# Kernel optimization log

Hardware: AMD Instinct MI355X
Metric: run time of the kernel (lower is better)

The kernel has to match this reference:

```python
import jax, jax.numpy as jnp
import numpy as np

# Config matching init_kwargs
DILS = [1, 3, 6, 12]          # flattened dilations for blocks [[1,3],[6,12]]
BLOCK_START = [0, 2]          # layer index where each block starts
IN = 64                       # input_size
SS = 256                      # state_size
HS = 128                      # h_size
OS = SS - HS                  # out_size for S2Cell
OUT = 8                       # output_size
B = 1024                      # batch (number of series)
T = 256                       # timesteps
# per-layer lxh input widths: [in, out, out+in, out] each + 2*h
IN_SIZES = [IN + 2 * HS, OS + 2 * HS, OS + IN + 2 * HS, OS + 2 * HS]


def setup_inputs() -> dict:
    key = jax.random.key(0)
    ks = jax.random.split(key, 12)
    d = {"x": jax.random.normal(ks[0], (T, B, IN), jnp.float32)}
    for i in range(4):
        fan_in = IN_SIZES[i]
        d[f"W{i}"] = jax.random.normal(ks[1 + i], (4 * SS, fan_in), jnp.float32) / np.sqrt(fan_in)
        d[f"b{i}"] = jnp.zeros((4 * SS,), jnp.float32)
    d["Wout"] = jax.random.normal(ks[9], (OUT, OS), jnp.float32) / np.sqrt(OS)
    d["bout"] = jnp.zeros((OUT,), jnp.float32)
    return d


def _s2cell(t, inp, W, b, prevH, prevC, bufH, bufC, dil):
    """One S2Cell step. bufH/bufC are circular buffers of length dil holding
    states from the last `dil` steps; bufH[t % dil] is the state from t-dil."""
    idx = t % dil
    has_del = t >= dil
    dH = jnp.where(has_del, bufH[idx], prevH)   # [B, HS]
    dC = bufC[idx]                               # [B, SS] (only used when has_del)
    xh = jnp.concatenate([inp, prevH, dH], axis=1)
    gates = xh @ W.T + b                         # [B, 4*SS]
    g0, g1, g2, g3 = jnp.split(gates, 4, axis=1)
    forget = jax.nn.sigmoid(g0 + 1.0)
    cand = jnp.tanh(g1)
    alpha = jax.nn.sigmoid(g2)
    out_gate = jax.nn.sigmoid(g3)
    weightedC = jnp.where(has_del, alpha * prevC + (1.0 - alpha) * dC, prevC)
    newC = jnp.where(t >= 1, forget * weightedC + (1.0 - forget) * cand, cand)
    whole = out_gate * newC                      # [B, SS]
    out_t, h = whole[:, :OS], whole[:, OS:]
    return out_t, h, newC, bufH.at[idx].set(h), bufC.at[idx].set(newC)


def reference(x, W0, b0, W1, b1, W2, b2, W3, b3, Wout, bout):
    Ws = [W0, W1, W2, W3]
    bs = [b0, b1, b2, b3]

    def init_layer(d):
        return (jnp.zeros((B, HS), x.dtype), jnp.zeros((B, SS), x.dtype),
                jnp.zeros((d, B, HS), x.dtype), jnp.zeros((d, B, SS), x.dtype))

    carry0 = (jnp.int32(0), tuple(init_layer(d) for d in DILS))

    def step(carry, x_t):
        t, states = carry
        new_states = []
        inp = x_t
        for li in range(4):
            if li in BLOCK_START and li > 0:
                # first layer of a later block: cat(previous block output, original input)
                inp = jnp.concatenate([inp, x_t], axis=1)
            prevH, prevC, bufH, bufC = states[li]
            inp, h, c, bufH, bufC = _s2cell(t, inp, Ws[li], bs[li], prevH, prevC, bufH, bufC, DILS[li])
            new_states.append((h, c, bufH, bufC))
        y = inp @ Wout.T + bout
        return (t + 1, tuple(new_states)), y

    _, ys = jax.lax.scan(step, carry0, x)
    return ys  # [T, B, OUT]
```

## Files before the change

kernel.cpp:

```cpp
#include <hip/hip_runtime.h>
#include <stdint.h>
#include <stdio.h>


typedef __attribute__((ext_vector_type(8))) short short8;
typedef __attribute__((ext_vector_type(4))) float f32x4;

#define DEVINL static __device__ __forceinline__

constexpr int TT = 256, BBATCH = 1024, INW = 64, HSW = 128, OSW = 128, NO = 8;
constexpr int ROWS = 128;

constexpr int KLa[4]   = {192, 384, 448, 384};
constexpr int DILa[4]  = {1, 3, 6, 12};
constexpr int PERa[4]  = {2, 4, 7, 13};
constexpr int LDWa[4]  = {200, 392, 456, 392};
constexpr int WOFFa[4] = {0, 6400, 18944, 33536};

constexpr int BIAS_B  = 46080 * 2;
constexpr int WOUT_B  = BIAS_B + 128 * 4;
constexpr int WSTR    = 129;
constexpr int BOUT_B  = WOUT_B + 8 * WSTR * 4;
constexpr int C3_B    = BOUT_B + 32;
constexpr int C3STR   = 132;
constexpr int LDS_BYTES = C3_B + 96 * C3STR * 4;

constexpr size_t WSBASE    = 8192;
constexpr size_t BH_OFF[4] = {0, 65536, 196608, 425984};
constexpr size_t OUTB_OFF  = 851968;
constexpr size_t CB_OFF    = 983040;
constexpr size_t C1_SZ     = 393216;
constexpr size_t C2_SZ     = 786432;
constexpr size_t CLSZ      = CB_OFF + C1_SZ + C2_SZ;
constexpr size_t WS_NEED   = WSBASE + 8 * CLSZ;

__host__ __device__ constexpr int seg_type(int L, int k) {
  if (L == 0) return k < 64 ? 0 : 2;
  if (L == 1) return k < 128 ? 1 : (k < 256 ? 2 : 3);
  if (L == 2) return k < 128 ? 1 : (k < 192 ? 0 : (k < 320 ? 2 : 3));
  return k < 128 ? 1 : (k < 256 ? 2 : 3);
}
__host__ __device__ constexpr int seg_start(int L, int k) {
  if (L == 0) return k < 64 ? 0 : 64;
  if (L == 1) return k < 128 ? 0 : (k < 256 ? 128 : 256);
  if (L == 2) return k < 128 ? 0 : (k < 192 ? 128 : (k < 320 ? 192 : 320));
  return k < 128 ? 0 : (k < 256 ? 128 : 256);
}

template <int N> struct IC { static constexpr int value = N; };

DEVINL unsigned short f2bf(float f) {
  union { float f; uint32_t u; } v; v.f = f;
  return (unsigned short)((v.u + 0x7FFFu + ((v.u >> 16) & 1u)) >> 16);
}
DEVINL float bf2f(unsigned short h) {
  union { uint32_t u; float f; } v; v.u = ((uint32_t)h) << 16;
  return v.f;
}
DEVINL float sigm(float x)  { return 1.0f / (1.0f + __expf(-x)); }
DEVINL float tanh_(float x) { return 1.0f - 2.0f / (__expf(2.0f * x) + 1.0f); }

DEVINL short8 zero_s8() { short8 v; for (int i = 0; i < 8; i++) v[i] = 0; return v; }
DEVINL f32x4  zero_f4() { f32x4  v; for (int i = 0; i < 4; i++) v[i] = 0.f; return v; }

DEVINL f32x4 mfma16(short8 a, short8 b, f32x4 c) {
  return __builtin_amdgcn_mfma_f32_16x16x32_bf16(a, b, c, 0, 0, 0);
}

DEVINL short8 ld8f(const float* p) {
  const f32x4 u0 = *(const f32x4*)p;
  const f32x4 u1 = *(const f32x4*)(p + 4);
  short8 r;
  r[0] = (short)f2bf(u0[0]); r[1] = (short)f2bf(u0[1]);
  r[2] = (short)f2bf(u0[2]); r[3] = (short)f2bf(u0[3]);
  r[4] = (short)f2bf(u1[0]); r[5] = (short)f2bf(u1[1]);
  r[6] = (short)f2bf(u1[2]); r[7] = (short)f2bf(u1[3]);
  return r;
}

__global__ void __launch_bounds__(256, 1)
rnn_stack_kernel(const float* __restrict__ x,
                 const float* __restrict__ W0, const float* __restrict__ b0,
                 const float* __restrict__ W1, const float* __restrict__ b1,
                 const float* __restrict__ W2, const float* __restrict__ b2,
                 const float* __restrict__ W3, const float* __restrict__ b3,
                 const float* __restrict__ Wout, const float* __restrict__ bout,
                 float* __restrict__ yout, char* __restrict__ ws)
{
  extern __shared__ char smem[];
  unsigned short* wlds = (unsigned short*)smem;
  float* biasl = (float*)(smem + BIAS_B);
  float* woutl = (float*)(smem + WOUT_B);
  float* boutl = (float*)(smem + BOUT_B);
  float* c3l   = (float*)(smem + C3_B);

  const int tid = threadIdx.x;

  __shared__ unsigned s_cg;
  if (tid == 0) {
    unsigned xcc;
    asm volatile("s_getreg_b32 %0, hwreg(HW_REG_XCC_ID)" : "=s"(xcc));
    xcc &= 7u;
    unsigned rank = __hip_atomic_fetch_add(
        (unsigned*)(ws + 4096 + (size_t)xcc * 64), 1u,
        __ATOMIC_RELAXED, __HIP_MEMORY_SCOPE_AGENT);
    s_cg = (xcc << 8) | (rank & 31u);
  }
  __syncthreads();
  const int c = __builtin_amdgcn_readfirstlane((int)(s_cg >> 8));
  const int g = __builtin_amdgcn_readfirstlane((int)(s_cg & 255));

  char* cb = ws + WSBASE + (size_t)c * CLSZ;
  unsigned short* bufH[4];
  unsigned short* outb[4];
#pragma unroll
  for (int l = 0; l < 4; l++) {
    bufH[l] = (unsigned short*)(cb + BH_OFF[l]);
    outb[l] = (unsigned short*)(cb + OUTB_OFF + (size_t)l * ROWS * OSW * 2);
  }
  float* bufC1 = (float*)(cb + CB_OFF + (size_t)g * (3 * 8 * ROWS * 4));
  float* bufC2 = (float*)(cb + CB_OFF + C1_SZ + (size_t)g * (6 * 8 * ROWS * 4));

  {
    const float* Wsrc[4] = {W0, W1, W2, W3};
    const float* bsrc[4] = {b0, b1, b2, b3};
    for (int l = 0; l < 4; l++) {
      const int K = KLa[l], LDW = LDWa[l];
      const int Ksrc = (l == 0) ? 320 : K;
      for (int n = 0; n < 32; n++) {
        const int grow = (n >> 3) * 256 + g * 8 + (n & 7);
        const float* src = Wsrc[l] + (size_t)grow * Ksrc;
        unsigned short* dst = wlds + WOFFa[l] + n * LDW;
        for (int k = tid; k < K; k += 256) {
          float v = src[k];
          if (l == 0 && k >= 64) v += src[k + 128];
          dst[k] = f2bf(v);
        }
      }
      if (tid < 32) biasl[l * 32 + tid] = bsrc[l][(tid >> 3) * 256 + g * 8 + (tid & 7)];
    }
    for (int i = tid; i < 8 * 128; i += 256) woutl[(i >> 7) * WSTR + (i & 127)] = Wout[i];
    if (tid < 8) boutl[tid] = bout[tid];
  }
  __syncthreads();

  const int wv = tid >> 6, lane = tid & 63, lm = lane & 15, quad = lane >> 4;
  const int m0 = wv * 32;
  const bool hi = lm >= 8;
  const int j = lm & 7;
  const int mrow = m0 + (hi ? 16 : 0) + quad * 4;

  unsigned* flg = (unsigned*)(ws + (size_t)c * 512 + (size_t)wv * 128);

  f32x4 pc[4];
#pragma unroll
  for (int l = 0; l < 4; l++) pc[l] = zero_f4();

  f32x4 acc00, acc01, acc10, acc11;

  auto arrive = [&](unsigned ep) {
    asm volatile("s_waitcnt vmcnt(0)" ::: "memory");
    if (lane == 0)
      __hip_atomic_store(flg + g, ep, __ATOMIC_RELAXED, __HIP_MEMORY_SCOPE_AGENT);
  };
  auto waitbar = [&](unsigned ep) {
    asm volatile("" ::: "memory");
    for (;;) {
      unsigned v = __hip_atomic_load(flg + (lane & 31), __ATOMIC_RELAXED,
                                     __HIP_MEMORY_SCOPE_AGENT);
      if (__all((int)(v >= ep))) break;
      __builtin_amdgcn_s_sleep(1);
    }
    asm volatile("buffer_inv sc0" ::: "memory");
  };

  auto pre = [&](auto Lc, int t) {
    constexpr int L = decltype(Lc)::value;
    constexpr int K = KLa[L];
    constexpr int NKT = K / 32;
    constexpr int DL = DILa[L];
    constexpr int P = PERa[L];
    constexpr int LDW = LDWa[L];
    const unsigned short* wl = wlds + WOFFa[L];
    const float bb0 = biasl[L * 32 + lm] + (lm < 8 ? 1.0f : 0.0f);
    const float bb1 = biasl[L * 32 + 16 + lm];
    acc00 = (f32x4){bb0, bb0, bb0, bb0};
    acc10 = acc00;
    acc01 = (f32x4){bb1, bb1, bb1, bb1};
    acc11 = acc01;
    const unsigned short* phb =
        (t >= 1) ? bufH[L] + (size_t)((t - 1) % P) * ROWS * HSW : nullptr;
    const unsigned short* dhb =
        (t >= DL) ? bufH[L] + (size_t)((t - DL) % P) * ROWS * HSW : phb;
    const float* xb = x + ((size_t)t * BBATCH + (size_t)c * ROWS) * INW;
#pragma unroll
    for (int kt = 0; kt < NKT; kt++) {
      const int sty = seg_type(L, kt * 32);
      if (sty == 1) continue;
      const int sst = seg_start(L, kt * 32);
      const int kloc = kt * 32 - sst + quad * 8;
      short8 a0, a1;
      if (sty == 0) {
        const float* p = xb + (size_t)(m0 + lm) * INW + kloc;
        a0 = ld8f(p);
        a1 = ld8f(p + 16 * INW);
      } else {
        const unsigned short* sb = (sty == 2) ? phb : dhb;
        if (sb) {
          const unsigned short* p = sb + (size_t)(m0 + lm) * HSW + kloc;
          a0 = *(const short8*)p;
          a1 = *(const short8*)(p + 16 * HSW);
        } else {
          a0 = zero_s8();
          a1 = zero_s8();
        }
      }
      const short8 bf0 = *(const short8*)(wl + (size_t)lm * LDW + kt * 32 + quad * 8);
      const short8 bf1 = *(const short8*)(wl + (size_t)(16 + lm) * LDW + kt * 32 + quad * 8);
      acc00 = mfma16(a0, bf0, acc00);
      acc01 = mfma16(a0, bf1, acc01);
      acc10 = mfma16(a1, bf0, acc10);
      acc11 = mfma16(a1, bf1, acc11);
    }
  };

  auto post = [&](auto Lc, int t) {
    constexpr int L = decltype(Lc)::value;
    constexpr int K = KLa[L];
    constexpr int NKT = K / 32;
    constexpr int DL = DILa[L];
    constexpr int P = PERa[L];
    constexpr int LDW = LDWa[L];
    if constexpr (L > 0) {
      const unsigned short* wl = wlds + WOFFa[L];
      const unsigned short* ob = outb[L - 1];
#pragma unroll
      for (int kt = 0; kt < NKT; kt++) {
        if (seg_type(L, kt * 32) != 1) continue;
        const int kloc = kt * 32 + quad * 8;
        const unsigned short* p = ob + (size_t)(m0 + lm) * HSW + kloc;
        const short8 a0 = *(const short8*)p;
        const short8 a1 = *(const short8*)(p + 16 * HSW);
        const short8 bf0 = *(const short8*)(wl + (size_t)lm * LDW + kt * 32 + quad * 8);
        const short8 bf1 = *(const short8*)(wl + (size_t)(16 + lm) * LDW + kt * 32 + quad * 8);
        acc00 = mfma16(a0, bf0, acc00);
        acc01 = mfma16(a0, bf1, acc01);
        acc10 = mfma16(a1, bf0, acc10);
        acc11 = mfma16(a1, bf1, acc11);
      }
    }
    f32x4 s00, s01, s10, s11;
#pragma unroll
    for (int r = 0; r < 4; r++) {
      s00[r] = __shfl_xor(acc00[r], 8);
      s01[r] = __shfl_xor(acc01[r], 8);
      s10[r] = __shfl_xor(acc10[r], 8);
      s11[r] = __shfl_xor(acc11[r], 8);
    }
    f32x4 G0, G1, G2, G3;
#pragma unroll
    for (int r = 0; r < 4; r++) {
      G0[r] = hi ? s10[r] : acc00[r];
      G1[r] = hi ? acc10[r] : s00[r];
      G2[r] = hi ? s11[r] : acc01[r];
      G3[r] = hi ? acc11[r] : s01[r];
    }
    float* cs = nullptr;
    if constexpr (L == 1) cs = bufC1 + ((size_t)(t % 3) * 8 + j) * ROWS + mrow;
    if constexpr (L == 2) cs = bufC2 + ((size_t)(t % 6) * 8 + j) * ROWS + mrow;
    float* cs3 = nullptr;
    if constexpr (L == 3) cs3 = c3l + ((size_t)(t % 12) * 8 + j) * C3STR + mrow;
    f32x4 dC = zero_f4();
    if constexpr (L == 1 || L == 2) { if (t >= DL) dC = *(const f32x4*)cs; }
    if constexpr (L == 3)           { if (t >= DL) dC = *(const f32x4*)cs3; }
    const f32x4 pcv = pc[L];
    f32x4 nC, wh;
#pragma unroll
    for (int q = 0; q < 4; q++) {
      const float fg = sigm(G0[q]);
      const float cd = tanh_(G1[q]);
      const float og = sigm(G3[q]);
      float wc;
      if constexpr (L == 0) {
        wc = pcv[q];
      } else {
        const float al = sigm(G2[q]);
        wc = (t >= DL) ? (al * pcv[q] + (1.0f - al) * dC[q]) : pcv[q];
      }
      const float nc = (t >= 1) ? (fg * wc + (1.0f - fg) * cd) : cd;
      nC[q] = nc;
      wh[q] = og * nc;
    }
    if constexpr (L == 1 || L == 2) *(f32x4*)cs = nC;
    if constexpr (L == 3)           *(f32x4*)cs3 = nC;
    pc[L] = nC;
    const int jg = g * 8 + j;
#pragma unroll
    for (int r = 0; r < 4; r++) {
      const unsigned short us = f2bf(wh[r]);
      const int row = mrow + r;
      if (g < 16) outb[L][(size_t)row * OSW + jg] = us;
      else bufH[L][((size_t)(t % P) * ROWS + row) * HSW + (jg - 128)] = us;
    }
  };

  auto epilogue = [&](int tt) {
    const int r = m0 + g;
    const unsigned short* orow = outb[3] + (size_t)r * OSW;
    const int o = lane >> 3, s = lane & 7;
    const short8 v0 = *(const short8*)(orow + s * 16);
    const short8 v1 = *(const short8*)(orow + s * 16 + 8);
    float part = 0.f;
#pragma unroll
    for (int i = 0; i < 8; i++)
      part += bf2f((unsigned short)v0[i]) * woutl[o * WSTR + s * 16 + i];
#pragma unroll
    for (int i = 0; i < 8; i++)
      part += bf2f((unsigned short)v1[i]) * woutl[o * WSTR + s * 16 + 8 + i];
    part += __shfl_down(part, 4);
    part += __shfl_down(part, 2);
    part += __shfl_down(part, 1);
    if (s == 0)
      yout[((size_t)tt * BBATCH + (size_t)c * ROWS + r) * NO + o] = part + boutl[o];
  };

  pre(IC<0>{}, 0);
  for (int t = 0; t < TT; t++) {
    const unsigned pb = 4u * t;
    post(IC<0>{}, t); arrive(pb + 1); pre(IC<1>{}, t);
    if (t > 0) epilogue(t - 1);
    waitbar(pb + 1);
    post(IC<1>{}, t); arrive(pb + 2); pre(IC<2>{}, t); waitbar(pb + 2);
    post(IC<2>{}, t); arrive(pb + 3); pre(IC<3>{}, t); waitbar(pb + 3);
    post(IC<3>{}, t); arrive(pb + 4);
    if (t + 1 < TT) pre(IC<0>{}, t + 1);
    waitbar(pb + 4);
  }
  epilogue(TT - 1);
}

extern "C" void kernel_launch(void* const* d_in, const int* in_sizes, int n_in,
                              void* d_out, int out_size, void* d_ws, size_t ws_size,
                              hipStream_t stream) {
  const float* x    = (const float*)d_in[0];
  const float* W0   = (const float*)d_in[1];
  const float* b0   = (const float*)d_in[2];
  const float* W1   = (const float*)d_in[3];
  const float* b1   = (const float*)d_in[4];
  const float* W2   = (const float*)d_in[5];
  const float* b2   = (const float*)d_in[6];
  const float* W3   = (const float*)d_in[7];
  const float* b3   = (const float*)d_in[8];
  const float* Wout = (const float*)d_in[9];
  const float* bout = (const float*)d_in[10];
  float* out = (float*)d_out;
  char* ws = (char*)d_ws;

  if (ws_size < WS_NEED) {
    fprintf(stderr, "kernel_launch: ws_size %zu < needed %zu\n", ws_size, (size_t)WS_NEED);
    return;
  }

  hipMemsetAsync(d_ws, 0, 8192, stream);

  hipError_t e = hipFuncSetAttribute((const void*)rnn_stack_kernel,
                                     hipFuncAttributeMaxDynamicSharedMemorySize,
                                     LDS_BYTES);
  if (e != hipSuccess) fprintf(stderr, "hipFuncSetAttribute: %d\n", (int)e);

  rnn_stack_kernel<<<dim3(256), dim3(256), LDS_BYTES, stream>>>(
      x, W0, b0, W1, b1, W2, b2, W3, b3, Wout, bout, out, ws);
  e = hipGetLastError();
  if (e != hipSuccess) fprintf(stderr, "launch error: %d\n", (int)e);
}
```

Baseline: 4.493 ms.

## Wavefront-pipeline layers across timesteps with one barrier per step

Replaces the four grid-wide barriers per timestep with a diagonal wavefront schedule. Layer L at step s processes timestep s-L, so all four layers run between a single barrier and cross-layer outputs are double-buffered by timestep parity. It also retiles the LDS weight layout into contiguous MFMA fragment blocks and changes the C-state buffers to per-thread contiguous float4 slots. Each barrier interval now carries more serial work, and the prologue and epilogue add three extra pipeline steps.

```diff
diff --git a/kernel.cpp b/kernel.cpp
--- a/kernel.cpp
+++ b/kernel.cpp
@@ -14,23 +14,22 @@
 constexpr int KLa[4]   = {192, 384, 448, 384};
 constexpr int DILa[4]  = {1, 3, 6, 12};
 constexpr int PERa[4]  = {2, 4, 7, 13};
-constexpr int LDWa[4]  = {200, 392, 456, 392};
-constexpr int WOFFa[4] = {0, 6400, 18944, 33536};
-
-constexpr int BIAS_B  = 46080 * 2;
-constexpr int WOUT_B  = BIAS_B + 128 * 4;
+constexpr int WOFFa[4] = {0, 6144, 18432, 32768};
+constexpr int WBYTES   = 90112;
+
+constexpr int BIAS_B  = WBYTES;
+constexpr int WOUT_B  = BIAS_B + 512;
 constexpr int WSTR    = 129;
 constexpr int BOUT_B  = WOUT_B + 8 * WSTR * 4;
 constexpr int C3_B    = BOUT_B + 32;
-constexpr int C3STR   = 132;
-constexpr int LDS_BYTES = C3_B + 96 * C3STR * 4;
+constexpr int LDS_BYTES = C3_B + 12 * 256 * 16;
 
 constexpr size_t WSBASE    = 8192;
 constexpr size_t BH_OFF[4] = {0, 65536, 196608, 425984};
 constexpr size_t OUTB_OFF  = 851968;
-constexpr size_t CB_OFF    = 983040;
-constexpr size_t C1_SZ     = 393216;
-constexpr size_t C2_SZ     = 786432;
+constexpr size_t CB_OFF    = OUTB_OFF + 8 * 32768;
+constexpr size_t C1_SZ     = 32 * 3 * 256 * 16;
+constexpr size_t C2_SZ     = 32 * 6 * 256 * 16;
 constexpr size_t CLSZ      = CB_OFF + C1_SZ + C2_SZ;
 constexpr size_t WS_NEED   = WSBASE + 8 * CLSZ;
 
@@ -112,29 +111,31 @@
 
   char* cb = ws + WSBASE + (size_t)c * CLSZ;
   unsigned short* bufH[4];
-  unsigned short* outb[4];
+  unsigned short* outb[8];
 #pragma unroll
   for (int l = 0; l < 4; l++) {
     bufH[l] = (unsigned short*)(cb + BH_OFF[l]);
-    outb[l] = (unsigned short*)(cb + OUTB_OFF + (size_t)l * ROWS * OSW * 2);
-  }
-  float* bufC1 = (float*)(cb + CB_OFF + (size_t)g * (3 * 8 * ROWS * 4));
-  float* bufC2 = (float*)(cb + CB_OFF + C1_SZ + (size_t)g * (6 * 8 * ROWS * 4));
+    outb[l * 2]     = (unsigned short*)(cb + OUTB_OFF + (size_t)(l * 2) * ROWS * OSW * 2);
+    outb[l * 2 + 1] = (unsigned short*)(cb + OUTB_OFF + (size_t)(l * 2 + 1) * ROWS * OSW * 2);
+  }
+  float* bufC1 = (float*)(cb + CB_OFF + (size_t)g * (3 * 256 * 16));
+  float* bufC2 = (float*)(cb + CB_OFF + C1_SZ + (size_t)g * (6 * 256 * 16));
 
   {
     const float* Wsrc[4] = {W0, W1, W2, W3};
     const float* bsrc[4] = {b0, b1, b2, b3};
     for (int l = 0; l < 4; l++) {
-      const int K = KLa[l], LDW = LDWa[l];
+      const int K = KLa[l];
       const int Ksrc = (l == 0) ? 320 : K;
+      unsigned short* base = wlds + WOFFa[l];
       for (int n = 0; n < 32; n++) {
         const int grow = (n >> 3) * 256 + g * 8 + (n & 7);
         const float* src = Wsrc[l] + (size_t)grow * Ksrc;
-        unsigned short* dst = wlds + WOFFa[l] + n * LDW;
         for (int k = tid; k < K; k += 256) {
           float v = src[k];
           if (l == 0 && k >= 64) v += src[k + 128];
-          dst[k] = f2bf(v);
+          base[((k >> 5) * 2 + (n >> 4)) * 512 + (n & 15) * 32 +
+               ((k >> 3) & 3) * 8 + (k & 7)] = f2bf(v);
         }
       }
       if (tid < 32) biasl[l * 32 + tid] = bsrc[l][(tid >> 3) * 256 + g * 8 + (tid & 7)];
@@ -155,8 +156,6 @@
   f32x4 pc[4];
 #pragma unroll
   for (int l = 0; l < 4; l++) pc[l] = zero_f4();
-
-  f32x4 acc00, acc01, acc10, acc11;
 
   auto arrive = [&](unsigned ep) {
     asm volatile("s_waitcnt vmcnt(0)" ::: "memory");
@@ -174,29 +173,35 @@
     asm volatile("buffer_inv sc0" ::: "memory");
   };
 
-  auto pre = [&](auto Lc, int t) {
+  auto do_layer = [&](auto Lc, int t) {
     constexpr int L = decltype(Lc)::value;
     constexpr int K = KLa[L];
     constexpr int NKT = K / 32;
     constexpr int DL = DILa[L];
     constexpr int P = PERa[L];
-    constexpr int LDW = LDWa[L];
+    if (t < 0 || t >= TT) return;
     const unsigned short* wl = wlds + WOFFa[L];
     const float bb0 = biasl[L * 32 + lm] + (lm < 8 ? 1.0f : 0.0f);
     const float bb1 = biasl[L * 32 + 16 + lm];
-    acc00 = (f32x4){bb0, bb0, bb0, bb0};
-    acc10 = acc00;
-    acc01 = (f32x4){bb1, bb1, bb1, bb1};
-    acc11 = acc01;
+    f32x4 acc00 = (f32x4){bb0, bb0, bb0, bb0};
+    f32x4 acc10 = acc00;
+    f32x4 acc01 = (f32x4){bb1, bb1, bb1, bb1};
+    f32x4 acc11 = acc01;
     const unsigned short* phb =
         (t >= 1) ? bufH[L] + (size_t)((t - 1) % P) * ROWS * HSW : nullptr;
     const unsigned short* dhb =
         (t >= DL) ? bufH[L] + (size_t)((t - DL) % P) * ROWS * HSW : phb;
+    const unsigned short* ob = (L > 0) ? outb[(L - 1) * 2 + (t & 1)] : nullptr;
     const float* xb = x + ((size_t)t * BBATCH + (size_t)c * ROWS) * INW;
+
+    f32x4 dC = zero_f4();
+    if constexpr (L == 1) { if (t >= DL) dC = *(const f32x4*)(bufC1 + ((size_t)(t % 3) * 256 + tid) * 4); }
+    if constexpr (L == 2) { if (t >= DL) dC = *(const f32x4*)(bufC2 + ((size_t)(t % 6) * 256 + tid) * 4); }
+    if constexpr (L == 3) { if (t >= DL) dC = *(const f32x4*)(c3l + ((size_t)(t % 12) * 256 + tid) * 4); }
+
 #pragma unroll
     for (int kt = 0; kt < NKT; kt++) {
       const int sty = seg_type(L, kt * 32);
-      if (sty == 1) continue;
       const int sst = seg_start(L, kt * 32);
       const int kloc = kt * 32 - sst + quad * 8;
       short8 a0, a1;
@@ -204,6 +209,10 @@
         const float* p = xb + (size_t)(m0 + lm) * INW + kloc;
         a0 = ld8f(p);
         a1 = ld8f(p + 16 * INW);
+      } else if (sty == 1) {
+        const unsigned short* p = ob + (size_t)(m0 + lm) * HSW + kloc;
+        a0 = *(const short8*)p;
+        a1 = *(const short8*)(p + 16 * HSW);
       } else {
         const unsigned short* sb = (sty == 2) ? phb : dhb;
         if (sb) {
@@ -215,39 +224,12 @@
           a1 = zero_s8();
         }
       }
-      const short8 bf0 = *(const short8*)(wl + (size_t)lm * LDW + kt * 32 + quad * 8);
-      const short8 bf1 = *(const short8*)(wl + (size_t)(16 + lm) * LDW + kt * 32 + quad * 8);
+      const short8 bf0 = *(const short8*)(wl + (kt * 2 + 0) * 512 + lm * 32 + quad * 8);
+      const short8 bf1 = *(const short8*)(wl + (kt * 2 + 1) * 512 + lm * 32 + quad * 8);
       acc00 = mfma16(a0, bf0, acc00);
       acc01 = mfma16(a0, bf1, acc01);
       acc10 = mfma16(a1, bf0, acc10);
       acc11 = mfma16(a1, bf1, acc11);
-    }
-  };
-
-  auto post = [&](auto Lc, int t) {
-    constexpr int L = decltype(Lc)::value;
-    constexpr int K = KLa[L];
-    constexpr int NKT = K / 32;
-    constexpr int DL = DILa[L];
-    constexpr int P = PERa[L];
-    constexpr int LDW = LDWa[L];
-    if constexpr (L > 0) {
-      const unsigned short* wl = wlds + WOFFa[L];
-      const unsigned short* ob = outb[L - 1];
-#pragma unroll
-      for (int kt = 0; kt < NKT; kt++) {
-        if (seg_type(L, kt * 32) != 1) continue;
-        const int kloc = kt * 32 + quad * 8;
-        const unsigned short* p = ob + (size_t)(m0 + lm) * HSW + kloc;
-        const short8 a0 = *(const short8*)p;
-        const short8 a1 = *(const short8*)(p + 16 * HSW);
-        const short8 bf0 = *(const short8*)(wl + (size_t)lm * LDW + kt * 32 + quad * 8);
-        const short8 bf1 = *(const short8*)(wl + (size_t)(16 + lm) * LDW + kt * 32 + quad * 8);
-        acc00 = mfma16(a0, bf0, acc00);
-        acc01 = mfma16(a0, bf1, acc01);
-        acc10 = mfma16(a1, bf0, acc10);
-        acc11 = mfma16(a1, bf1, acc11);
-      }
     }
     f32x4 s00, s01, s10, s11;
 #pragma unroll
@@ -265,14 +247,6 @@
       G2[r] = hi ? s11[r] : acc01[r];
       G3[r] = hi ? acc11[r] : s01[r];
     }
-    float* cs = nullptr;
-    if constexpr (L == 1) cs = bufC1 + ((size_t)(t % 3) * 8 + j) * ROWS + mrow;
-    if constexpr (L == 2) cs = bufC2 + ((size_t)(t % 6) * 8 + j) * ROWS + mrow;
-    float* cs3 = nullptr;
-    if constexpr (L == 3) cs3 = c3l + ((size_t)(t % 12) * 8 + j) * C3STR + mrow;
-    f32x4 dC = zero_f4();
-    if constexpr (L == 1 || L == 2) { if (t >= DL) dC = *(const f32x4*)cs; }
-    if constexpr (L == 3)           { if (t >= DL) dC = *(const f32x4*)cs3; }
     const f32x4 pcv = pc[L];
     f32x4 nC, wh;
 #pragma unroll
@@ -291,22 +265,24 @@
       nC[q] = nc;
       wh[q] = og * nc;
     }
-    if constexpr (L == 1 || L == 2) *(f32x4*)cs = nC;
-    if constexpr (L == 3)           *(f32x4*)cs3 = nC;
+    if constexpr (L == 1) *(f32x4*)(bufC1 + ((size_t)(t % 3) * 256 + tid) * 4) = nC;
+    if constexpr (L == 2) *(f32x4*)(bufC2 + ((size_t)(t % 6) * 256 + tid) * 4) = nC;
+    if constexpr (L == 3) *(f32x4*)(c3l + ((size_t)(t % 12) * 256 + tid) * 4) = nC;
     pc[L] = nC;
     const int jg = g * 8 + j;
+    unsigned short* outw = outb[L * 2 + (t & 1)];
 #pragma unroll
     for (int r = 0; r < 4; r++) {
       const unsigned short us = f2bf(wh[r]);
       const int row = mrow + r;
-      if (g < 16) outb[L][(size_t)row * OSW + jg] = us;
+      if (g < 16) outw[(size_t)row * OSW + jg] = us;
       else bufH[L][((size_t)(t % P) * ROWS + row) * HSW + (jg - 128)] = us;
     }
   };
 
   auto epilogue = [&](int tt) {
     const int r = m0 + g;
-    const unsigned short* orow = outb[3] + (size_t)r * OSW;
+    const unsigned short* orow = outb[3 * 2 + (tt & 1)] + (size_t)r * OSW;
     const int o = lane >> 3, s = lane & 7;
     const short8 v0 = *(const short8*)(orow + s * 16);
     const short8 v1 = *(const short8*)(orow + s * 16 + 8);
@@ -324,17 +300,14 @@
       yout[((size_t)tt * BBATCH + (size_t)c * ROWS + r) * NO + o] = part + boutl[o];
   };
 
-  pre(IC<0>{}, 0);
-  for (int t = 0; t < TT; t++) {
-    const unsigned pb = 4u * t;
-    post(IC<0>{}, t); arrive(pb + 1); pre(IC<1>{}, t);
-    if (t > 0) epilogue(t - 1);
-    waitbar(pb + 1);
-    post(IC<1>{}, t); arrive(pb + 2); pre(IC<2>{}, t); waitbar(pb + 2);
-    post(IC<2>{}, t); arrive(pb + 3); pre(IC<3>{}, t); waitbar(pb + 3);
-    post(IC<3>{}, t); arrive(pb + 4);
-    if (t + 1 < TT) pre(IC<0>{}, t + 1);
-    waitbar(pb + 4);
+  for (int s = 0; s < TT + 3; s++) {
+    do_layer(IC<0>{}, s);
+    do_layer(IC<1>{}, s - 1);
+    do_layer(IC<2>{}, s - 2);
+    do_layer(IC<3>{}, s - 3);
+    if (s >= 4) epilogue(s - 4);
+    arrive((unsigned)(s + 1));
+    waitbar((unsigned)(s + 1));
   }
   epilogue(TT - 1);
 }
```

Result: slower. 5.641 ms (+25.5%).

## Double waves per block, split rows per wave and swizzle LDS weight layout

Applied to the files above, without the earlier changes.

Launches 512 threads per block instead of 256, so each wave owns 16 batch rows instead of 32 and issues half the MFMAs per step. This shortens the serial per-step critical path. Weights are stored in LDS in an MFMA-fragment-tiled layout rather than a padded row-major layout, and the cell-state buffers are reorganised into per-lane float4 slots. The A fragments and the delayed C are loaded up front, and the gate math now runs only on half the lanes. In exchange the grid barrier has more waves to synchronise and flag polling, and half the lanes sit idle during the elementwise step.

```diff
diff --git a/kernel.cpp b/kernel.cpp
--- a/kernel.cpp
+++ b/kernel.cpp
@@ -14,23 +14,22 @@
 constexpr int KLa[4]   = {192, 384, 448, 384};
 constexpr int DILa[4]  = {1, 3, 6, 12};
 constexpr int PERa[4]  = {2, 4, 7, 13};
-constexpr int LDWa[4]  = {200, 392, 456, 392};
-constexpr int WOFFa[4] = {0, 6400, 18944, 33536};
-
-constexpr int BIAS_B  = 46080 * 2;
-constexpr int WOUT_B  = BIAS_B + 128 * 4;
+constexpr int WOFFa[4] = {0, 6144, 18432, 32768};
+constexpr int WBYTES   = 90112;
+
+constexpr int BIAS_B  = WBYTES;
+constexpr int WOUT_B  = BIAS_B + 512;
 constexpr int WSTR    = 129;
 constexpr int BOUT_B  = WOUT_B + 8 * WSTR * 4;
 constexpr int C3_B    = BOUT_B + 32;
-constexpr int C3STR   = 132;
-constexpr int LDS_BYTES = C3_B + 96 * C3STR * 4;
-
-constexpr size_t WSBASE    = 8192;
+constexpr int LDS_BYTES = C3_B + 12 * 256 * 16;
+
+constexpr size_t WSBASE    = 16384;
 constexpr size_t BH_OFF[4] = {0, 65536, 196608, 425984};
 constexpr size_t OUTB_OFF  = 851968;
 constexpr size_t CB_OFF    = 983040;
-constexpr size_t C1_SZ     = 393216;
-constexpr size_t C2_SZ     = 786432;
+constexpr size_t C1_SZ     = 32 * 3 * 256 * 16;
+constexpr size_t C2_SZ     = 32 * 6 * 256 * 16;
 constexpr size_t CLSZ      = CB_OFF + C1_SZ + C2_SZ;
 constexpr size_t WS_NEED   = WSBASE + 8 * CLSZ;
 
@@ -78,7 +77,7 @@
   return r;
 }
 
-__global__ void __launch_bounds__(256, 1)
+__global__ void __launch_bounds__(512, 1)
 rnn_stack_kernel(const float* __restrict__ x,
                  const float* __restrict__ W0, const float* __restrict__ b0,
                  const float* __restrict__ W1, const float* __restrict__ b1,
@@ -102,7 +101,7 @@
     asm volatile("s_getreg_b32 %0, hwreg(HW_REG_XCC_ID)" : "=s"(xcc));
     xcc &= 7u;
     unsigned rank = __hip_atomic_fetch_add(
-        (unsigned*)(ws + 4096 + (size_t)xcc * 64), 1u,
+        (unsigned*)(ws + 8192 + (size_t)xcc * 64), 1u,
         __ATOMIC_RELAXED, __HIP_MEMORY_SCOPE_AGENT);
     s_cg = (xcc << 8) | (rank & 31u);
   }
@@ -118,45 +117,47 @@
     bufH[l] = (unsigned short*)(cb + BH_OFF[l]);
     outb[l] = (unsigned short*)(cb + OUTB_OFF + (size_t)l * ROWS * OSW * 2);
   }
-  float* bufC1 = (float*)(cb + CB_OFF + (size_t)g * (3 * 8 * ROWS * 4));
-  float* bufC2 = (float*)(cb + CB_OFF + C1_SZ + (size_t)g * (6 * 8 * ROWS * 4));
+  float* bufC1 = (float*)(cb + CB_OFF + (size_t)g * (3 * 256 * 16));
+  float* bufC2 = (float*)(cb + CB_OFF + C1_SZ + (size_t)g * (6 * 256 * 16));
 
   {
     const float* Wsrc[4] = {W0, W1, W2, W3};
     const float* bsrc[4] = {b0, b1, b2, b3};
     for (int l = 0; l < 4; l++) {
-      const int K = KLa[l], LDW = LDWa[l];
+      const int K = KLa[l];
       const int Ksrc = (l == 0) ? 320 : K;
+      unsigned short* base = wlds + WOFFa[l];
       for (int n = 0; n < 32; n++) {
         const int grow = (n >> 3) * 256 + g * 8 + (n & 7);
         const float* src = Wsrc[l] + (size_t)grow * Ksrc;
-        unsigned short* dst = wlds + WOFFa[l] + n * LDW;
-        for (int k = tid; k < K; k += 256) {
+        for (int k = tid; k < K; k += 512) {
           float v = src[k];
           if (l == 0 && k >= 64) v += src[k + 128];
-          dst[k] = f2bf(v);
+          base[((k >> 5) * 2 + (n >> 4)) * 512 + (n & 15) * 32 +
+               ((k >> 3) & 3) * 8 + (k & 7)] = f2bf(v);
         }
       }
       if (tid < 32) biasl[l * 32 + tid] = bsrc[l][(tid >> 3) * 256 + g * 8 + (tid & 7)];
     }
-    for (int i = tid; i < 8 * 128; i += 256) woutl[(i >> 7) * WSTR + (i & 127)] = Wout[i];
+    for (int i = tid; i < 8 * 128; i += 512) woutl[(i >> 7) * WSTR + (i & 127)] = Wout[i];
     if (tid < 8) boutl[tid] = bout[tid];
   }
   __syncthreads();
 
   const int wv = tid >> 6, lane = tid & 63, lm = lane & 15, quad = lane >> 4;
-  const int m0 = wv * 32;
-  const bool hi = lm >= 8;
+  const int m0 = wv * 16;
   const int j = lm & 7;
-  const int mrow = m0 + (hi ? 16 : 0) + quad * 4;
-
-  unsigned* flg = (unsigned*)(ws + (size_t)c * 512 + (size_t)wv * 128);
+  const int mrow = m0 + quad * 4;
+  const int oid = wv * 32 + quad * 8 + j;
+
+  unsigned* flg = (unsigned*)(ws + (size_t)c * 1024 + (size_t)wv * 128);
 
   f32x4 pc[4];
 #pragma unroll
   for (int l = 0; l < 4; l++) pc[l] = zero_f4();
 
-  f32x4 acc00, acc01, acc10, acc11;
+  f32x4 acc0, acc1;
+  f32x4 dCreg = zero_f4();
 
   auto arrive = [&](unsigned ep) {
     asm volatile("s_waitcnt vmcnt(0)" ::: "memory");
@@ -180,132 +181,107 @@
     constexpr int NKT = K / 32;
     constexpr int DL = DILa[L];
     constexpr int P = PERa[L];
-    constexpr int LDW = LDWa[L];
     const unsigned short* wl = wlds + WOFFa[L];
     const float bb0 = biasl[L * 32 + lm] + (lm < 8 ? 1.0f : 0.0f);
     const float bb1 = biasl[L * 32 + 16 + lm];
-    acc00 = (f32x4){bb0, bb0, bb0, bb0};
-    acc10 = acc00;
-    acc01 = (f32x4){bb1, bb1, bb1, bb1};
-    acc11 = acc01;
+    acc0 = (f32x4){bb0, bb0, bb0, bb0};
+    acc1 = (f32x4){bb1, bb1, bb1, bb1};
+    dCreg = zero_f4();
+    if constexpr (L == 1) { if (t >= DL) dCreg = *(const f32x4*)(bufC1 + ((size_t)(t % 3) * 256 + oid) * 4); }
+    if constexpr (L == 2) { if (t >= DL) dCreg = *(const f32x4*)(bufC2 + ((size_t)(t % 6) * 256 + oid) * 4); }
+    if constexpr (L == 3) { if (t >= DL) dCreg = *(const f32x4*)(c3l + ((size_t)(t % 12) * 256 + oid) * 4); }
     const unsigned short* phb =
         (t >= 1) ? bufH[L] + (size_t)((t - 1) % P) * ROWS * HSW : nullptr;
     const unsigned short* dhb =
         (t >= DL) ? bufH[L] + (size_t)((t - DL) % P) * ROWS * HSW : phb;
     const float* xb = x + ((size_t)t * BBATCH + (size_t)c * ROWS) * INW;
+    short8 af[NKT];
 #pragma unroll
     for (int kt = 0; kt < NKT; kt++) {
       const int sty = seg_type(L, kt * 32);
       if (sty == 1) continue;
       const int sst = seg_start(L, kt * 32);
       const int kloc = kt * 32 - sst + quad * 8;
-      short8 a0, a1;
       if (sty == 0) {
-        const float* p = xb + (size_t)(m0 + lm) * INW + kloc;
-        a0 = ld8f(p);
-        a1 = ld8f(p + 16 * INW);
+        af[kt] = ld8f(xb + (size_t)(m0 + lm) * INW + kloc);
       } else {
         const unsigned short* sb = (sty == 2) ? phb : dhb;
-        if (sb) {
-          const unsigned short* p = sb + (size_t)(m0 + lm) * HSW + kloc;
-          a0 = *(const short8*)p;
-          a1 = *(const short8*)(p + 16 * HSW);
-        } else {
-          a0 = zero_s8();
-          a1 = zero_s8();
-        }
-      }
-      const short8 bf0 = *(const short8*)(wl + (size_t)lm * LDW + kt * 32 + quad * 8);
-      const short8 bf1 = *(const short8*)(wl + (size_t)(16 + lm) * LDW + kt * 32 + quad * 8);
-      acc00 = mfma16(a0, bf0, acc00);
-      acc01 = mfma16(a0, bf1, acc01);
-      acc10 = mfma16(a1, bf0, acc10);
-      acc11 = mfma16(a1, bf1, acc11);
+        af[kt] = sb ? *(const short8*)(sb + (size_t)(m0 + lm) * HSW + kloc)
+                    : zero_s8();
+      }
+    }
+#pragma unroll
+    for (int kt = 0; kt < NKT; kt++) {
+      if (seg_type(L, kt * 32) == 1) continue;
+      const short8 bf0v = *(const short8*)(wl + (kt * 2 + 0) * 512 + lm * 32 + quad * 8);
+      const short8 bf1v = *(const short8*)(wl + (kt * 2 + 1) * 512 + lm * 32 + quad * 8);
+      acc0 = mfma16(af[kt], bf0v, acc0);
+      acc1 = mfma16(af[kt], bf1v, acc1);
     }
   };
 
   auto post = [&](auto Lc, int t) {
     constexpr int L = decltype(Lc)::value;
-    constexpr int K = KLa[L];
-    constexpr int NKT = K / 32;
     constexpr int DL = DILa[L];
     constexpr int P = PERa[L];
-    constexpr int LDW = LDWa[L];
     if constexpr (L > 0) {
       const unsigned short* wl = wlds + WOFFa[L];
       const unsigned short* ob = outb[L - 1];
-#pragma unroll
-      for (int kt = 0; kt < NKT; kt++) {
-        if (seg_type(L, kt * 32) != 1) continue;
-        const int kloc = kt * 32 + quad * 8;
-        const unsigned short* p = ob + (size_t)(m0 + lm) * HSW + kloc;
-        const short8 a0 = *(const short8*)p;
-        const short8 a1 = *(const short8*)(p + 16 * HSW);
-        const short8 bf0 = *(const short8*)(wl + (size_t)lm * LDW + kt * 32 + quad * 8);
-        const short8 bf1 = *(const short8*)(wl + (size_t)(16 + lm) * LDW + kt * 32 + quad * 8);
-        acc00 = mfma16(a0, bf0, acc00);
-        acc01 = mfma16(a0, bf1, acc01);
-        acc10 = mfma16(a1, bf0, acc10);
-        acc11 = mfma16(a1, bf1, acc11);
-      }
-    }
-    f32x4 s00, s01, s10, s11;
+      short8 af2[4];
+#pragma unroll
+      for (int kt = 0; kt < 4; kt++)
+        af2[kt] = *(const short8*)(ob + (size_t)(m0 + lm) * HSW + kt * 32 + quad * 8);
+#pragma unroll
+      for (int kt = 0; kt < 4; kt++) {
+        const short8 bf0v = *(const short8*)(wl + (kt * 2 + 0) * 512 + lm * 32 + quad * 8);
+        const short8 bf1v = *(const short8*)(wl + (kt * 2 + 1) * 512 + lm * 32 + quad * 8);
+        acc0 = mfma16(af2[kt], bf0v, acc0);
+        acc1 = mfma16(af2[kt], bf1v, acc1);
+      }
+    }
+    f32x4 s0, s1;
 #pragma unroll
     for (int r = 0; r < 4; r++) {
-      s00[r] = __shfl_xor(acc00[r], 8);
-      s01[r] = __shfl_xor(acc01[r], 8);
-      s10[r] = __shfl_xor(acc10[r], 8);
-      s11[r] = __shfl_xor(acc11[r], 8);
-    }
-    f32x4 G0, G1, G2, G3;
-#pragma unroll
-    for (int r = 0; r < 4; r++) {
-      G0[r] = hi ? s10[r] : acc00[r];
-      G1[r] = hi ? acc10[r] : s00[r];
-      G2[r] = hi ? s11[r] : acc01[r];
-      G3[r] = hi ? acc11[r] : s01[r];
-    }
-    float* cs = nullptr;
-    if constexpr (L == 1) cs = bufC1 + ((size_t)(t % 3) * 8 + j) * ROWS + mrow;
-    if constexpr (L == 2) cs = bufC2 + ((size_t)(t % 6) * 8 + j) * ROWS + mrow;
-    float* cs3 = nullptr;
-    if constexpr (L == 3) cs3 = c3l + ((size_t)(t % 12) * 8 + j) * C3STR + mrow;
-    f32x4 dC = zero_f4();
-    if constexpr (L == 1 || L == 2) { if (t >= DL) dC = *(const f32x4*)cs; }
-    if constexpr (L == 3)           { if (t >= DL) dC = *(const f32x4*)cs3; }
-    const f32x4 pcv = pc[L];
-    f32x4 nC, wh;
-#pragma unroll
-    for (int q = 0; q < 4; q++) {
-      const float fg = sigm(G0[q]);
-      const float cd = tanh_(G1[q]);
-      const float og = sigm(G3[q]);
-      float wc;
-      if constexpr (L == 0) {
-        wc = pcv[q];
-      } else {
-        const float al = sigm(G2[q]);
-        wc = (t >= DL) ? (al * pcv[q] + (1.0f - al) * dC[q]) : pcv[q];
-      }
-      const float nc = (t >= 1) ? (fg * wc + (1.0f - fg) * cd) : cd;
-      nC[q] = nc;
-      wh[q] = og * nc;
-    }
-    if constexpr (L == 1 || L == 2) *(f32x4*)cs = nC;
-    if constexpr (L == 3)           *(f32x4*)cs3 = nC;
-    pc[L] = nC;
-    const int jg = g * 8 + j;
-#pragma unroll
-    for (int r = 0; r < 4; r++) {
-      const unsigned short us = f2bf(wh[r]);
-      const int row = mrow + r;
-      if (g < 16) outb[L][(size_t)row * OSW + jg] = us;
-      else bufH[L][((size_t)(t % P) * ROWS + row) * HSW + (jg - 128)] = us;
+      s0[r] = __shfl_xor(acc0[r], 8);
+      s1[r] = __shfl_xor(acc1[r], 8);
+    }
+    if (lm < 8) {
+      const f32x4 G0 = acc0, G1 = s0, G2 = acc1, G3 = s1;
+      const f32x4 pcv = pc[L];
+      f32x4 nC, wh;
+#pragma unroll
+      for (int q = 0; q < 4; q++) {
+        const float fg = sigm(G0[q]);
+        const float cd = tanh_(G1[q]);
+        const float og = sigm(G3[q]);
+        float wc;
+        if constexpr (L == 0) {
+          wc = pcv[q];
+        } else {
+          const float al = sigm(G2[q]);
+          wc = (t >= DL) ? (al * pcv[q] + (1.0f - al) * dCreg[q]) : pcv[q];
+        }
+        const float nc = (t >= 1) ? (fg * wc + (1.0f - fg) * cd) : cd;
+        nC[q] = nc;
+        wh[q] = og * nc;
+      }
+      if constexpr (L == 1) *(f32x4*)(bufC1 + ((size_t)(t % 3) * 256 + oid) * 4) = nC;
+      if constexpr (L == 2) *(f32x4*)(bufC2 + ((size_t)(t % 6) * 256 + oid) * 4) = nC;
+      if constexpr (L == 3) *(f32x4*)(c3l + ((size_t)(t % 12) * 256 + oid) * 4) = nC;
+      pc[L] = nC;
+      const int jg = g * 8 + j;
+#pragma unroll
+      for (int r = 0; r < 4; r++) {
+        const unsigned short us = f2bf(wh[r]);
+        const int row = mrow + r;
+        if (g < 16) outb[L][(size_t)row * OSW + jg] = us;
+        else bufH[L][((size_t)(t % P) * ROWS + row) * HSW + (jg - 128)] = us;
+      }
     }
   };
 
   auto epilogue = [&](int tt) {
-    const int r = m0 + g;
+    const int r = m0 + (g & 15);
     const unsigned short* orow = outb[3] + (size_t)r * OSW;
     const int o = lane >> 3, s = lane & 7;
     const short8 v0 = *(const short8*)(orow + s * 16);
@@ -361,14 +337,14 @@
     return;
   }
 
-  hipMemsetAsync(d_ws, 0, 8192, stream);
+  hipMemsetAsync(d_ws, 0, 16384, stream);
 
   hipError_t e = hipFuncSetAttribute((const void*)rnn_stack_kernel,
                                      hipFuncAttributeMaxDynamicSharedMemorySize,
                                      LDS_BYTES);
   if (e != hipSuccess) fprintf(stderr, "hipFuncSetAttribute: %d\n", (int)e);
 
-  rnn_stack_kernel<<<dim3(256), dim3(256), LDS_BYTES, stream>>>(
+  rnn_stack_kernel<<<dim3(256), dim3(512), LDS_BYTES, stream>>>(
       x, W0, b0, W1, b1, W2, b2, W3, b3, Wout, bout, out, ws);
   e = hipGetLastError();
   if (e != hipSuccess) fprintf(stderr, "launch error: %d\n", (int)e);
```

Measured after the change: 6.347 ms. 1.41x slower.
